# Performance work log

Measured on AMD Instinct MI355X. Metric: run time of the kernel, lower is better.

Reference implementation:

```python
import jax, jax.numpy as jnp
import numpy as np

N_NODES = 50000
N_EDGES = 600000
IN_F, HID, OUT_F = 602, 128, 41


def _gconv(x, W, b, src, dst, n):
    # DGL GraphConv, norm='both': D_dst^{-1/2} A (D_src^{-1/2} x W) + b
    ones = jnp.ones(src.shape, dtype=x.dtype)
    deg_out = jnp.clip(jax.ops.segment_sum(ones, src, num_segments=n), 1.0)
    deg_in = jnp.clip(jax.ops.segment_sum(ones, dst, num_segments=n), 1.0)
    h = x * jax.lax.rsqrt(deg_out)[:, None]
    h = h @ W  # dense transform first (in_feats > out_feats path)
    agg = jax.ops.segment_sum(h[src], dst, num_segments=n)  # [N, out]
    return agg * jax.lax.rsqrt(deg_in)[:, None] + b


def setup_inputs() -> dict:
    key = jax.random.key(0)
    ks = jax.random.split(key, 8)
    features = jax.random.normal(ks[0], (N_NODES, IN_F), dtype=jnp.float32)
    src = jax.random.randint(ks[1], (N_EDGES,), 0, N_NODES, dtype=jnp.int32)
    dst = jax.random.randint(ks[2], (N_EDGES,), 0, N_NODES, dtype=jnp.int32)
    def glorot(k, fan_in, fan_out):
        s = jnp.sqrt(6.0 / (fan_in + fan_out)).astype(jnp.float32)
        return jax.random.uniform(k, (fan_in, fan_out), jnp.float32, -s, s)
    return {
        'features': features, 'src': src, 'dst': dst,
        'W1': glorot(ks[3], IN_F, HID), 'b1': jnp.zeros((HID,), jnp.float32),
        'W2': glorot(ks[4], HID, HID), 'b2': jnp.zeros((HID,), jnp.float32),
        'W3': glorot(ks[5], HID, HID), 'b3': jnp.zeros((HID,), jnp.float32),
        'Wfc': glorot(ks[6], HID, OUT_F), 'bfc': jnp.zeros((OUT_F,), jnp.float32),
    }


def reference(features, src, dst, W1, b1, W2, b2, W3, b3, Wfc, bfc):
    n = features.shape[0]
    relu = jax.nn.relu
    x = relu(_gconv(features, W1, b1, src, dst, n))  # x = _x
    _x = relu(_gconv(x, W2, b2, src, dst, n))        # branch (layer2)
    x = relu(_gconv(x, W2, b2, src, dst, n))         # main (same layer2)
    x = relu(_gconv(x, W3, b3, src, dst, n))         # layer3
    x = relu(x + _x)                                  # residual + relu
    return x @ Wfc + bfc
```

## Files before the change

### kernel.cpp

```cpp
#include <hip/hip_runtime.h>
#include <hip/hip_bf16.h>

#define NN   50000
#define NE   600000
#define INF  602
#define HID  128
#define OUTF 41
#define NBLK 196

typedef __attribute__((ext_vector_type(8))) short bf16x8;
typedef __attribute__((ext_vector_type(4))) float f32x4;

__device__ inline unsigned short f2bf(float x) {
    unsigned u = __float_as_uint(x);
    unsigned r = u + 0x7FFF + ((u >> 16) & 1);
    return (unsigned short)(r >> 16);
}

#define GLL16(gp, lp) \
    __builtin_amdgcn_global_load_lds((const __attribute__((address_space(1))) unsigned int*)(gp), \
                                     (__attribute__((address_space(3))) unsigned int*)(lp), 16, 0, 0)

__global__ __launch_bounds__(256) void deg_hist_k(const int* __restrict__ src,
                                                  const int* __restrict__ dst,
                                                  int* __restrict__ cnt_out,
                                                  int* __restrict__ cnt_in, int E) {
    int e = blockIdx.x * 256 + threadIdx.x;
    if (e < E) {
        atomicAdd(&cnt_out[src[e]], 1);
        atomicAdd(&cnt_in[dst[e]], 1);
    }
}

__global__ __launch_bounds__(256) void scan1_k(const int* __restrict__ cnt,
                                               int* __restrict__ rowptr,
                                               int* __restrict__ blockSum) {
    __shared__ int tmp[256];
    int tid = threadIdx.x;
    int i = blockIdx.x * 256 + tid;
    int v = (i < NN) ? cnt[i] : 0;
    tmp[tid] = v;
    __syncthreads();
#pragma unroll
    for (int off = 1; off < 256; off <<= 1) {
        int t = (tid >= off) ? tmp[tid - off] : 0;
        __syncthreads();
        tmp[tid] += t;
        __syncthreads();
    }
    if (i < NN) rowptr[i] = tmp[tid] - v;
    if (tid == 255) blockSum[blockIdx.x] = tmp[255];
}

__global__ __launch_bounds__(256) void scan2_k(const int* __restrict__ blockSum,
                                               int* __restrict__ blockOff,
                                               int* __restrict__ rowptr) {
    __shared__ int tmp[256];
    int tid = threadIdx.x;
    int v = (tid < NBLK) ? blockSum[tid] : 0;
    tmp[tid] = v;
    __syncthreads();
#pragma unroll
    for (int off = 1; off < 256; off <<= 1) {
        int t = (tid >= off) ? tmp[tid - off] : 0;
        __syncthreads();
        tmp[tid] += t;
        __syncthreads();
    }
    if (tid < NBLK) blockOff[tid] = tmp[tid] - v;
    if (tid == 255) rowptr[NN] = tmp[255];
}

__global__ __launch_bounds__(256) void scan3_k(int* __restrict__ rowptr,
                                               const int* __restrict__ blockOff,
                                               int* __restrict__ wcur,
                                               const int* __restrict__ cnt_out,
                                               const int* __restrict__ cnt_in,
                                               float* __restrict__ rs_out,
                                               float* __restrict__ rs_in) {
    int i = blockIdx.x * 256 + threadIdx.x;
    if (i < NN) {
        int r = rowptr[i] + blockOff[blockIdx.x];
        rowptr[i] = r;
        wcur[i] = r;
        int co = cnt_out[i]; if (co < 1) co = 1;
        int ci = cnt_in[i];  if (ci < 1) ci = 1;
        rs_out[i] = rsqrtf((float)co);
        rs_in[i]  = rsqrtf((float)ci);
    }
}

__global__ __launch_bounds__(256) void fill_csr_k(const int* __restrict__ src,
                                                  const int* __restrict__ dst,
                                                  int* __restrict__ wcur,
                                                  int* __restrict__ csrsrc, int E) {
    int e = blockIdx.x * 256 + threadIdx.x;
    if (e < E) {
        int p = atomicAdd(&wcur[dst[e]], 1);
        csrsrc[p] = src[e];
    }
}

__device__ inline void prep_w_body(const float* __restrict__ W, int K,
                                   unsigned short* __restrict__ out, int total4, int i) {
    if (i >= total4) return;
    int col = i & 127;
    int k4 = (i >> 7) << 2;
    short4 h;
    h.x = (short)f2bf((k4 + 0 < K) ? W[(size_t)(k4 + 0) * HID + col] : 0.f);
    h.y = (short)f2bf((k4 + 1 < K) ? W[(size_t)(k4 + 1) * HID + col] : 0.f);
    h.z = (short)f2bf((k4 + 2 < K) ? W[(size_t)(k4 + 2) * HID + col] : 0.f);
    h.w = (short)f2bf((k4 + 3 < K) ? W[(size_t)(k4 + 3) * HID + col] : 0.f);
    *(short4*)&out[(size_t)(k4 >> 3) * 1024 + col * 8 + (k4 & 7)] = h;
}

__global__ __launch_bounds__(256) void prep_w_k(const float* __restrict__ W, int K,
                                                unsigned short* __restrict__ out, int total4) {
    prep_w_body(W, K, out, total4, blockIdx.x * 256 + threadIdx.x);
}

__global__ __launch_bounds__(256) void prep_w2_k(const float* __restrict__ Wa,
                                                 unsigned short* __restrict__ outa,
                                                 const float* __restrict__ Wb,
                                                 unsigned short* __restrict__ outb) {
    if (blockIdx.x < 16)
        prep_w_body(Wa, HID, outa, 4096, blockIdx.x * 256 + threadIdx.x);
    else
        prep_w_body(Wb, HID, outb, 4096, (blockIdx.x - 16) * 256 + threadIdx.x);
}

__global__ __launch_bounds__(256) void gemm1_k(const float* __restrict__ A,
                                               const unsigned short* __restrict__ Wt,
                                               const float* __restrict__ rs_out,
                                               unsigned short* __restrict__ H, int n) {
    __shared__ __attribute__((aligned(16))) short As[64 * 136];
    __shared__ __attribute__((aligned(16))) short Bs[16 * 1024];

    const int tid = threadIdx.x;
    const int wave = tid >> 6;
    const int lane = tid & 63;
    const int quad = lane >> 4;
    const int l16 = lane & 15;
    const int rowBase = blockIdx.x * 64;
    const int tileBase = rowBase + wave * 16;

    float4 apf[8];
    auto loadA = [&](int ch) {
        int kb = ch * 128;
#pragma unroll
        for (int c = 0; c < 8; ++c) {
            int f = c * 256 + tid;
            int row = f >> 5;
            int kc = (f & 31) << 2;
            int grow = rowBase + row;
            int gk = kb + kc;
            float4 v = {0.f, 0.f, 0.f, 0.f};
            if (grow < n) {
                if (gk + 3 < INF) {
                    v = *(const float4*)(A + (size_t)grow * INF + gk);
                } else {
                    if (gk + 0 < INF) v.x = A[(size_t)grow * INF + gk + 0];
                    if (gk + 1 < INF) v.y = A[(size_t)grow * INF + gk + 1];
                    if (gk + 2 < INF) v.z = A[(size_t)grow * INF + gk + 2];
                }
            }
            apf[c] = v;
        }
    };
    auto storeA = [&]() {
#pragma unroll
        for (int c = 0; c < 8; ++c) {
            int f = c * 256 + tid;
            int row = f >> 5;
            int kc = (f & 31) << 2;
            short4 h;
            h.x = (short)f2bf(apf[c].x); h.y = (short)f2bf(apf[c].y);
            h.z = (short)f2bf(apf[c].z); h.w = (short)f2bf(apf[c].w);
            *(short4*)&As[row * 136 + kc] = h;
        }
    };
    auto issueB = [&](int ch) {
#pragma unroll
        for (int c = 0; c < 8; ++c)
            GLL16(Wt + (size_t)ch * 16384 + c * 2048 + tid * 8, &Bs[c * 2048 + tid * 8]);
    };

    f32x4 acc[8];
#pragma unroll
    for (int j = 0; j < 8; ++j) acc[j] = (f32x4){0.f, 0.f, 0.f, 0.f};

    loadA(0);
    for (int ch = 0; ch < 5; ++ch) {
        __syncthreads();
        issueB(ch);
        storeA();
        __syncthreads();
        if (ch + 1 < 5) loadA(ch + 1);
#pragma unroll
        for (int s = 0; s < 4; ++s) {
            bf16x8 af = *(const bf16x8*)&As[(wave * 16 + l16) * 136 + s * 32 + quad * 8];
            const short* bg = &Bs[(s * 4 + quad) * 1024 + l16 * 8];
#pragma unroll
            for (int nt = 0; nt < 8; ++nt) {
                bf16x8 bf = *(const bf16x8*)(bg + nt * 128);
                acc[nt] = __builtin_amdgcn_mfma_f32_16x16x32_bf16(af, bf, acc[nt], 0, 0, 0);
            }
        }
    }

#pragma unroll
    for (int r = 0; r < 4; ++r) {
        int row = tileBase + quad * 4 + r;
        if (row < n) {
            float ro = rs_out[row];
#pragma unroll
            for (int nt = 0; nt < 8; ++nt)
                H[(size_t)row * HID + nt * 16 + l16] = f2bf(acc[nt][r] * ro);
        }
    }
}

__global__ __launch_bounds__(256) void gemm_hid_k(const unsigned short* __restrict__ A,
                                                  const unsigned short* __restrict__ Wt,
                                                  unsigned short* __restrict__ H, int n) {
    __shared__ __attribute__((aligned(16))) short As[64 * 136];
    __shared__ __attribute__((aligned(16))) short Bs[16384];

    const int tid = threadIdx.x;
    const int wave = tid >> 6;
    const int lane = tid & 63;
    const int quad = lane >> 4;
    const int l16 = lane & 15;
    const int wm = wave >> 1;
    const int wn = wave & 1;
    const int rowBase = blockIdx.x * 64;

#pragma unroll
    for (int c = 0; c < 8; ++c)
        GLL16(Wt + c * 2048 + tid * 8, &Bs[c * 2048 + tid * 8]);

#pragma unroll
    for (int c = 0; c < 4; ++c) {
        int f = c * 256 + tid;
        int row = f >> 4;
        int k16 = (f & 15) << 3;
        int grow = rowBase + row;
        int4 v = {0, 0, 0, 0};
        if (grow < n) v = *(const int4*)(A + (size_t)grow * HID + k16);
        *(int4*)&As[row * 136 + k16] = v;
    }
    __syncthreads();

    f32x4 acc[2][4];
#pragma unroll
    for (int i = 0; i < 2; ++i)
#pragma unroll
        for (int j = 0; j < 4; ++j) acc[i][j] = (f32x4){0.f, 0.f, 0.f, 0.f};

#pragma unroll
    for (int kq = 0; kq < 4; ++kq) {
        bf16x8 af[2], bfr[4];
#pragma unroll
        for (int mt = 0; mt < 2; ++mt)
            af[mt] = *(const bf16x8*)&As[(wm * 32 + mt * 16 + l16) * 136 + kq * 32 + quad * 8];
#pragma unroll
        for (int nt = 0; nt < 4; ++nt)
            bfr[nt] = *(const bf16x8*)&Bs[(kq * 4 + quad) * 1024 + (wn * 64 + nt * 16 + l16) * 8];
#pragma unroll
        for (int mt = 0; mt < 2; ++mt)
#pragma unroll
            for (int nt = 0; nt < 4; ++nt)
                acc[mt][nt] = __builtin_amdgcn_mfma_f32_16x16x32_bf16(af[mt], bfr[nt], acc[mt][nt], 0, 0, 0);
    }

#pragma unroll
    for (int mt = 0; mt < 2; ++mt)
#pragma unroll
        for (int r = 0; r < 4; ++r) {
            int row = rowBase + wm * 32 + mt * 16 + quad * 4 + r;
            if (row < n) {
#pragma unroll
                for (int nt = 0; nt < 4; ++nt) {
                    int col = wn * 64 + nt * 16 + l16;
                    H[(size_t)row * HID + col] = f2bf(acc[mt][nt][r]);
                }
            }
        }
}

__global__ __launch_bounds__(256) void gather_k(const unsigned short* __restrict__ H,
                                                const int* __restrict__ rowptr,
                                                const int* __restrict__ csrsrc,
                                                const float* __restrict__ rs_in,
                                                const float* __restrict__ rs_out,
                                                const float* __restrict__ bias,
                                                const float* __restrict__ resid,
                                                float* __restrict__ outX,
                                                unsigned short* __restrict__ outXs,
                                                int n) {
    const int lane = threadIdx.x & 63;
    const int g = lane >> 4;
    const int l = lane & 15;
    const int gbase = g << 4;
    const int wid = blockIdx.x * 4 + (threadIdx.x >> 6);
    const int node = wid * 4 + g;
    const bool alive = node < n;

    int beg = 0, end = 0;
    if (alive) { beg = rowptr[node]; end = rowptr[node + 1]; }

    float acc[8];
#pragma unroll
    for (int k = 0; k < 8; ++k) acc[k] = 0.f;

    auto accum = [&](int s) {
        int4 u = *(const int4*)(H + (size_t)s * HID + l * 8);
        unsigned x = (unsigned)u.x, y = (unsigned)u.y, z = (unsigned)u.z, w = (unsigned)u.w;
        acc[0] += __uint_as_float(x << 16); acc[1] += __uint_as_float(x & 0xFFFF0000u);
        acc[2] += __uint_as_float(y << 16); acc[3] += __uint_as_float(y & 0xFFFF0000u);
        acc[4] += __uint_as_float(z << 16); acc[5] += __uint_as_float(z & 0xFFFF0000u);
        acc[6] += __uint_as_float(w << 16); acc[7] += __uint_as_float(w & 0xFFFF0000u);
    };

    for (int base = beg; base < end; base += 16) {
        int m = end - base; if (m > 16) m = 16;
        int idx = (l < m) ? csrsrc[base + l] : 0;
        int j = 0;
        for (; j + 3 < m; j += 4) {
            int s0 = __shfl(idx, gbase | j);
            int s1 = __shfl(idx, gbase | (j + 1));
            int s2 = __shfl(idx, gbase | (j + 2));
            int s3 = __shfl(idx, gbase | (j + 3));
            int4 u0 = *(const int4*)(H + (size_t)s0 * HID + l * 8);
            int4 u1 = *(const int4*)(H + (size_t)s1 * HID + l * 8);
            int4 u2 = *(const int4*)(H + (size_t)s2 * HID + l * 8);
            int4 u3 = *(const int4*)(H + (size_t)s3 * HID + l * 8);
#pragma unroll
            for (int q = 0; q < 4; ++q) {
                int4 u = (q == 0) ? u0 : (q == 1) ? u1 : (q == 2) ? u2 : u3;
                unsigned x = (unsigned)u.x, y = (unsigned)u.y, z = (unsigned)u.z, w = (unsigned)u.w;
                acc[0] += __uint_as_float(x << 16); acc[1] += __uint_as_float(x & 0xFFFF0000u);
                acc[2] += __uint_as_float(y << 16); acc[3] += __uint_as_float(y & 0xFFFF0000u);
                acc[4] += __uint_as_float(z << 16); acc[5] += __uint_as_float(z & 0xFFFF0000u);
                acc[6] += __uint_as_float(w << 16); acc[7] += __uint_as_float(w & 0xFFFF0000u);
            }
        }
        for (; j < m; ++j) accum(__shfl(idx, gbase | j));
    }

    if (!alive) return;

    float ri = rs_in[node];
    float4 b0 = *(const float4*)(bias + l * 8);
    float4 b1 = *(const float4*)(bias + l * 8 + 4);
    float v[8];
    v[0] = fmaxf(acc[0] * ri + b0.x, 0.f); v[1] = fmaxf(acc[1] * ri + b0.y, 0.f);
    v[2] = fmaxf(acc[2] * ri + b0.z, 0.f); v[3] = fmaxf(acc[3] * ri + b0.w, 0.f);
    v[4] = fmaxf(acc[4] * ri + b1.x, 0.f); v[5] = fmaxf(acc[5] * ri + b1.y, 0.f);
    v[6] = fmaxf(acc[6] * ri + b1.z, 0.f); v[7] = fmaxf(acc[7] * ri + b1.w, 0.f);

    size_t o = (size_t)node * HID + l * 8;
    if (resid) {
        float4 r0 = *(const float4*)(resid + o);
        float4 r1 = *(const float4*)(resid + o + 4);
        v[0] = fmaxf(v[0] + r0.x, 0.f); v[1] = fmaxf(v[1] + r0.y, 0.f);
        v[2] = fmaxf(v[2] + r0.z, 0.f); v[3] = fmaxf(v[3] + r0.w, 0.f);
        v[4] = fmaxf(v[4] + r1.x, 0.f); v[5] = fmaxf(v[5] + r1.y, 0.f);
        v[6] = fmaxf(v[6] + r1.z, 0.f); v[7] = fmaxf(v[7] + r1.w, 0.f);
    }
    if (outX) {
        *(float4*)(outX + o) = make_float4(v[0], v[1], v[2], v[3]);
        *(float4*)(outX + o + 4) = make_float4(v[4], v[5], v[6], v[7]);
    }
    if (outXs) {
        float ro = rs_out[node];
        int4 h;
        h.x = (int)(((unsigned)f2bf(v[1] * ro) << 16) | f2bf(v[0] * ro));
        h.y = (int)(((unsigned)f2bf(v[3] * ro) << 16) | f2bf(v[2] * ro));
        h.z = (int)(((unsigned)f2bf(v[5] * ro) << 16) | f2bf(v[4] * ro));
        h.w = (int)(((unsigned)f2bf(v[7] * ro) << 16) | f2bf(v[6] * ro));
        *(int4*)(outXs + o) = h;
    }
}

__global__ __launch_bounds__(256) void fc_k(const float* __restrict__ X,
                                            const float* __restrict__ Wfc,
                                            const float* __restrict__ bfc,
                                            float* __restrict__ out, int n) {
    __shared__ float Ws[HID * OUTF];
    __shared__ float Xs[4][HID];
    int tid = threadIdx.x;
    for (int i = tid; i < HID * OUTF; i += 256) Ws[i] = Wfc[i];
    int rowBase = blockIdx.x * 4;
    for (int i = tid; i < 4 * HID; i += 256) {
        int r = i >> 7, c = i & 127;
        int gr = rowBase + r;
        Xs[r][c] = (gr < n) ? X[(size_t)gr * HID + c] : 0.f;
    }
    __syncthreads();
    int wv = tid >> 6, lane = tid & 63;
    int row = rowBase + wv;
    if (row < n && lane < OUTF) {
        float acc = bfc[lane];
#pragma unroll 8
        for (int k = 0; k < HID; ++k) acc += Xs[wv][k] * Ws[k * OUTF + lane];
        out[(size_t)row * OUTF + lane] = acc;
    }
}

extern "C" void kernel_launch(void* const* d_in, const int* in_sizes, int n_in,
                              void* d_out, int out_size, void* d_ws, size_t ws_size,
                              hipStream_t stream) {
    const float* feat = (const float*)d_in[0];
    const int* src = (const int*)d_in[1];
    const int* dst = (const int*)d_in[2];
    const float* W1 = (const float*)d_in[3];
    const float* b1 = (const float*)d_in[4];
    const float* W2 = (const float*)d_in[5];
    const float* b2 = (const float*)d_in[6];
    const float* W3 = (const float*)d_in[7];
    const float* b3 = (const float*)d_in[8];
    const float* Wfc = (const float*)d_in[9];
    const float* bfc = (const float*)d_in[10];
    float* out = (float*)d_out;

    char* w = (char*)d_ws;
    auto alloc = [&](size_t b) -> void* {
        void* p = (void*)w;
        w += (b + 255) & ~(size_t)255;
        return p;
    };
    int* cnt = (int*)alloc(2 * NN * sizeof(int));
    int* cnt_out = cnt;
    int* cnt_in  = cnt + NN;
    int* rowptr  = (int*)alloc((NN + 1) * sizeof(int));
    int* wcur    = (int*)alloc(NN * sizeof(int));
    int* csrsrc  = (int*)alloc(NE * sizeof(int));
    int* blockSum = (int*)alloc(NBLK * sizeof(int));
    int* blockOff = (int*)alloc(NBLK * sizeof(int));
    float* rs_out = (float*)alloc(NN * sizeof(float));
    float* rs_in  = (float*)alloc(NN * sizeof(float));
    unsigned short* W1t = (unsigned short*)alloc(10 * 8192 * sizeof(unsigned short));
    unsigned short* W2t = (unsigned short*)alloc(16384 * sizeof(unsigned short));
    unsigned short* W3t = (unsigned short*)alloc(16384 * sizeof(unsigned short));
    unsigned short* Hb = (unsigned short*)alloc((size_t)NN * HID * sizeof(unsigned short));
    unsigned short* Xb = (unsigned short*)alloc((size_t)NN * HID * sizeof(unsigned short));
    float* resid = (float*)alloc((size_t)NN * HID * sizeof(float));
    float* Xfc   = (float*)alloc((size_t)NN * HID * sizeof(float));

    hipMemsetAsync(cnt, 0, 2 * NN * sizeof(int), stream);

    prep_w_k<<<80, 256, 0, stream>>>(W1, INF, W1t, 20480);
    prep_w2_k<<<32, 256, 0, stream>>>(W2, W2t, W3, W3t);

    deg_hist_k<<<(NE + 255) / 256, 256, 0, stream>>>(src, dst, cnt_out, cnt_in, NE);
    scan1_k<<<NBLK, 256, 0, stream>>>(cnt_in, rowptr, blockSum);
    scan2_k<<<1, 256, 0, stream>>>(blockSum, blockOff, rowptr);
    scan3_k<<<NBLK, 256, 0, stream>>>(rowptr, blockOff, wcur, cnt_out, cnt_in, rs_out, rs_in);
    fill_csr_k<<<(NE + 255) / 256, 256, 0, stream>>>(src, dst, wcur, csrsrc, NE);

    const int gblk = (NN + 63) / 64;
    const int ablk = (NN + 15) / 16;
    gemm1_k<<<gblk, 256, 0, stream>>>(feat, W1t, rs_out, Hb, NN);
    gather_k<<<ablk, 256, 0, stream>>>(Hb, rowptr, csrsrc, rs_in, rs_out, b1,
                                       nullptr, nullptr, Xb, NN);
    gemm_hid_k<<<gblk, 256, 0, stream>>>(Xb, W2t, Hb, NN);
    gather_k<<<ablk, 256, 0, stream>>>(Hb, rowptr, csrsrc, rs_in, rs_out, b2,
                                       nullptr, resid, Xb, NN);
    gemm_hid_k<<<gblk, 256, 0, stream>>>(Xb, W3t, Hb, NN);
    gather_k<<<ablk, 256, 0, stream>>>(Hb, rowptr, csrsrc, rs_in, rs_out, b3,
                                       resid, Xfc, nullptr, NN);
    fc_k<<<(NN + 3) / 4, 256, 0, stream>>>(Xfc, Wfc, bfc, out, NN);
}
```

Measured before the change: 455.7 us.

## Fuse neighbor gather into following GEMM and final FC; merge scan and prep kernels

Each gather/aggregation stage is fused with the next dense transform. The aggregated, normalized bf16 rows are written straight into the GEMM's LDS tile instead of round-tripping through global memory. The last gather is fused with the residual add and the 41-wide FC layer, which drops the fp32 Xfc buffer. The two-level scan's second and third kernels are merged, with each block reducing blockSum itself, and the weight prep and memset are merged into one kernel, cutting launches. The costs are lower parallelism in the gather phase (64 rows per block, 4 passes per wave) and more LDS per block, which may lower occupancy.

```diff
diff --git a/kernel.cpp b/kernel.cpp
--- a/kernel.cpp
+++ b/kernel.cpp
@@ -52,35 +52,30 @@
     if (tid == 255) blockSum[blockIdx.x] = tmp[255];
 }
 
-__global__ __launch_bounds__(256) void scan2_k(const int* __restrict__ blockSum,
-                                               int* __restrict__ blockOff,
-                                               int* __restrict__ rowptr) {
-    __shared__ int tmp[256];
-    int tid = threadIdx.x;
-    int v = (tid < NBLK) ? blockSum[tid] : 0;
-    tmp[tid] = v;
+__global__ __launch_bounds__(256) void scan23_k(int* __restrict__ rowptr,
+                                                const int* __restrict__ blockSum,
+                                                int* __restrict__ wcur,
+                                                const int* __restrict__ cnt_out,
+                                                const int* __restrict__ cnt_in,
+                                                float* __restrict__ rs_out,
+                                                float* __restrict__ rs_in) {
+    const int tid = threadIdx.x;
+    const int bid = blockIdx.x;
+    int vAll = (tid < NBLK) ? blockSum[tid] : 0;
+    int vPre = (tid < bid) ? vAll : 0;
+#pragma unroll
+    for (int o = 32; o; o >>= 1) {
+        vAll += __shfl_down(vAll, o);
+        vPre += __shfl_down(vPre, o);
+    }
+    __shared__ int sA[4], sP[4];
+    if ((tid & 63) == 0) { sA[tid >> 6] = vAll; sP[tid >> 6] = vPre; }
     __syncthreads();
-#pragma unroll
-    for (int off = 1; off < 256; off <<= 1) {
-        int t = (tid >= off) ? tmp[tid - off] : 0;
-        __syncthreads();
-        tmp[tid] += t;
-        __syncthreads();
-    }
-    if (tid < NBLK) blockOff[tid] = tmp[tid] - v;
-    if (tid == 255) rowptr[NN] = tmp[255];
-}
-
-__global__ __launch_bounds__(256) void scan3_k(int* __restrict__ rowptr,
-                                               const int* __restrict__ blockOff,
-                                               int* __restrict__ wcur,
-                                               const int* __restrict__ cnt_out,
-                                               const int* __restrict__ cnt_in,
-                                               float* __restrict__ rs_out,
-                                               float* __restrict__ rs_in) {
-    int i = blockIdx.x * 256 + threadIdx.x;
+    int offAll = sA[0] + sA[1] + sA[2] + sA[3];
+    int offPre = sP[0] + sP[1] + sP[2] + sP[3];
+    int i = bid * 256 + tid;
     if (i < NN) {
-        int r = rowptr[i] + blockOff[blockIdx.x];
+        int r = rowptr[i] + offPre;
         rowptr[i] = r;
         wcur[i] = r;
         int co = cnt_out[i]; if (co < 1) co = 1;
@@ -88,6 +83,7 @@
         rs_out[i] = rsqrtf((float)co);
         rs_in[i]  = rsqrtf((float)ci);
     }
+    if (bid == NBLK - 1 && tid == 0) rowptr[NN] = offAll;
 }
 
 __global__ __launch_bounds__(256) void fill_csr_k(const int* __restrict__ src,
@@ -114,19 +110,23 @@
     *(short4*)&out[(size_t)(k4 >> 3) * 1024 + col * 8 + (k4 & 7)] = h;
 }
 
-__global__ __launch_bounds__(256) void prep_w_k(const float* __restrict__ W, int K,
-                                                unsigned short* __restrict__ out, int total4) {
-    prep_w_body(W, K, out, total4, blockIdx.x * 256 + threadIdx.x);
-}
-
-__global__ __launch_bounds__(256) void prep_w2_k(const float* __restrict__ Wa,
-                                                 unsigned short* __restrict__ outa,
-                                                 const float* __restrict__ Wb,
-                                                 unsigned short* __restrict__ outb) {
-    if (blockIdx.x < 16)
-        prep_w_body(Wa, HID, outa, 4096, blockIdx.x * 256 + threadIdx.x);
-    else
-        prep_w_body(Wb, HID, outb, 4096, (blockIdx.x - 16) * 256 + threadIdx.x);
+__global__ __launch_bounds__(256) void prep_all_k(const float* __restrict__ W1,
+                                                  const float* __restrict__ W2,
+                                                  const float* __restrict__ W3,
+                                                  unsigned short* __restrict__ W1t,
+                                                  unsigned short* __restrict__ W2t,
+                                                  unsigned short* __restrict__ W3t,
+                                                  int* __restrict__ cnt) {
+    int b = blockIdx.x;
+    if (b < 80) {
+        int t = b * 256 + threadIdx.x;
+        prep_w_body(W1, INF, W1t, 20480, t);
+        for (int i = t; i < 2 * NN; i += 20480) cnt[i] = 0;
+    } else if (b < 96) {
+        prep_w_body(W2, HID, W2t, 4096, (b - 80) * 256 + threadIdx.x);
+    } else {
+        prep_w_body(W3, HID, W3t, 4096, (b - 96) * 256 + threadIdx.x);
+    }
 }
 
 __global__ __launch_bounds__(256) void gemm1_k(const float* __restrict__ A,
@@ -220,124 +220,68 @@
     }
 }
 
-__global__ __launch_bounds__(256) void gemm_hid_k(const unsigned short* __restrict__ A,
-                                                  const unsigned short* __restrict__ Wt,
-                                                  unsigned short* __restrict__ H, int n) {
+__global__ __launch_bounds__(256) void fgath_gemm_k(const unsigned short* __restrict__ Hin,
+                                                    const unsigned short* __restrict__ Wt,
+                                                    const int* __restrict__ rowptr,
+                                                    const int* __restrict__ csrsrc,
+                                                    const float* __restrict__ rs_in,
+                                                    const float* __restrict__ rs_out,
+                                                    const float* __restrict__ bias,
+                                                    float* __restrict__ resid,
+                                                    unsigned short* __restrict__ Hout,
+                                                    int n) {
     __shared__ __attribute__((aligned(16))) short As[64 * 136];
     __shared__ __attribute__((aligned(16))) short Bs[16384];
 
     const int tid = threadIdx.x;
     const int wave = tid >> 6;
     const int lane = tid & 63;
-    const int quad = lane >> 4;
-    const int l16 = lane & 15;
-    const int wm = wave >> 1;
-    const int wn = wave & 1;
-    const int rowBase = blockIdx.x * 64;
-
-#pragma unroll
-    for (int c = 0; c < 8; ++c)
-        GLL16(Wt + c * 2048 + tid * 8, &Bs[c * 2048 + tid * 8]);
-
-#pragma unroll
-    for (int c = 0; c < 4; ++c) {
-        int f = c * 256 + tid;
-        int row = f >> 4;
-        int k16 = (f & 15) << 3;
-        int grow = rowBase + row;
-        int4 v = {0, 0, 0, 0};
-        if (grow < n) v = *(const int4*)(A + (size_t)grow * HID + k16);
-        *(int4*)&As[row * 136 + k16] = v;
-    }
-    __syncthreads();
-
-    f32x4 acc[2][4];
-#pragma unroll
-    for (int i = 0; i < 2; ++i)
-#pragma unroll
-        for (int j = 0; j < 4; ++j) acc[i][j] = (f32x4){0.f, 0.f, 0.f, 0.f};
-
-#pragma unroll
-    for (int kq = 0; kq < 4; ++kq) {
-        bf16x8 af[2], bfr[4];
-#pragma unroll
-        for (int mt = 0; mt < 2; ++mt)
-            af[mt] = *(const bf16x8*)&As[(wm * 32 + mt * 16 + l16) * 136 + kq * 32 + quad * 8];
-#pragma unroll
-        for (int nt = 0; nt < 4; ++nt)
-            bfr[nt] = *(const bf16x8*)&Bs[(kq * 4 + quad) * 1024 + (wn * 64 + nt * 16 + l16) * 8];
-#pragma unroll
-        for (int mt = 0; mt < 2; ++mt)
-#pragma unroll
-            for (int nt = 0; nt < 4; ++nt)
-                acc[mt][nt] = __builtin_amdgcn_mfma_f32_16x16x32_bf16(af[mt], bfr[nt], acc[mt][nt], 0, 0, 0);
-    }
-
-#pragma unroll
-    for (int mt = 0; mt < 2; ++mt)
-#pragma unroll
-        for (int r = 0; r < 4; ++r) {
-            int row = rowBase + wm * 32 + mt * 16 + quad * 4 + r;
-            if (row < n) {
-#pragma unroll
-                for (int nt = 0; nt < 4; ++nt) {
-                    int col = wn * 64 + nt * 16 + l16;
-                    H[(size_t)row * HID + col] = f2bf(acc[mt][nt][r]);
-                }
-            }
-        }
-}
-
-__global__ __launch_bounds__(256) void gather_k(const unsigned short* __restrict__ H,
-                                                const int* __restrict__ rowptr,
-                                                const int* __restrict__ csrsrc,
-                                                const float* __restrict__ rs_in,
-                                                const float* __restrict__ rs_out,
-                                                const float* __restrict__ bias,
-                                                const float* __restrict__ resid,
-                                                float* __restrict__ outX,
-                                                unsigned short* __restrict__ outXs,
-                                                int n) {
-    const int lane = threadIdx.x & 63;
     const int g = lane >> 4;
     const int l = lane & 15;
     const int gbase = g << 4;
-    const int wid = blockIdx.x * 4 + (threadIdx.x >> 6);
-    const int node = wid * 4 + g;
-    const bool alive = node < n;
-
-    int beg = 0, end = 0;
-    if (alive) { beg = rowptr[node]; end = rowptr[node + 1]; }
-
-    float acc[8];
-#pragma unroll
-    for (int k = 0; k < 8; ++k) acc[k] = 0.f;
-
-    auto accum = [&](int s) {
-        int4 u = *(const int4*)(H + (size_t)s * HID + l * 8);
-        unsigned x = (unsigned)u.x, y = (unsigned)u.y, z = (unsigned)u.z, w = (unsigned)u.w;
-        acc[0] += __uint_as_float(x << 16); acc[1] += __uint_as_float(x & 0xFFFF0000u);
-        acc[2] += __uint_as_float(y << 16); acc[3] += __uint_as_float(y & 0xFFFF0000u);
-        acc[4] += __uint_as_float(z << 16); acc[5] += __uint_as_float(z & 0xFFFF0000u);
-        acc[6] += __uint_as_float(w << 16); acc[7] += __uint_as_float(w & 0xFFFF0000u);
-    };
-
-    for (int base = beg; base < end; base += 16) {
-        int m = end - base; if (m > 16) m = 16;
-        int idx = (l < m) ? csrsrc[base + l] : 0;
-        int j = 0;
-        for (; j + 3 < m; j += 4) {
-            int s0 = __shfl(idx, gbase | j);
-            int s1 = __shfl(idx, gbase | (j + 1));
-            int s2 = __shfl(idx, gbase | (j + 2));
-            int s3 = __shfl(idx, gbase | (j + 3));
-            int4 u0 = *(const int4*)(H + (size_t)s0 * HID + l * 8);
-            int4 u1 = *(const int4*)(H + (size_t)s1 * HID + l * 8);
-            int4 u2 = *(const int4*)(H + (size_t)s2 * HID + l * 8);
-            int4 u3 = *(const int4*)(H + (size_t)s3 * HID + l * 8);
-#pragma unroll
-            for (int q = 0; q < 4; ++q) {
-                int4 u = (q == 0) ? u0 : (q == 1) ? u1 : (q == 2) ? u2 : u3;
+    const int rowBase = blockIdx.x * 64;
+
+#pragma unroll
+    for (int c = 0; c < 8; ++c)
+        GLL16(Wt + c * 2048 + tid * 8, &Bs[c * 2048 + tid * 8]);
+
+    for (int p = 0; p < 4; ++p) {
+        int lrow = wave * 16 + p * 4 + g;
+        int node = rowBase + lrow;
+        bool alive = node < n;
+        int beg = 0, end = 0;
+        if (alive) { beg = rowptr[node]; end = rowptr[node + 1]; }
+
+        float acc[8];
+#pragma unroll
+        for (int k = 0; k < 8; ++k) acc[k] = 0.f;
+
+        for (int base = beg; base < end; base += 16) {
+            int m = end - base; if (m > 16) m = 16;
+            int idx = (l < m) ? csrsrc[base + l] : 0;
+            int j = 0;
+            for (; j + 3 < m; j += 4) {
+                int s0 = __shfl(idx, gbase | j);
+                int s1 = __shfl(idx, gbase | (j + 1));
+                int s2 = __shfl(idx, gbase | (j + 2));
+                int s3 = __shfl(idx, gbase | (j + 3));
+                int4 u0 = *(const int4*)(Hin + (size_t)s0 * HID + l * 8);
+                int4 u1 = *(const int4*)(Hin + (size_t)s1 * HID + l * 8);
+                int4 u2 = *(const int4*)(Hin + (size_t)s2 * HID + l * 8);
+                int4 u3 = *(const int4*)(Hin + (size_t)s3 * HID + l * 8);
+#pragma unroll
+                for (int q = 0; q < 4; ++q) {
+                    int4 u = (q == 0) ? u0 : (q == 1) ? u1 : (q == 2) ? u2 : u3;
+                    unsigned x = (unsigned)u.x, y = (unsigned)u.y, z = (unsigned)u.z, w = (unsigned)u.w;
+                    acc[0] += __uint_as_float(x << 16); acc[1] += __uint_as_float(x & 0xFFFF0000u);
+                    acc[2] += __uint_as_float(y << 16); acc[3] += __uint_as_float(y & 0xFFFF0000u);
+                    acc[4] += __uint_as_float(z << 16); acc[5] += __uint_as_float(z & 0xFFFF0000u);
+                    acc[6] += __uint_as_float(w << 16); acc[7] += __uint_as_float(w & 0xFFFF0000u);
+                }
+            }
+            for (; j < m; ++j) {
+                int s = __shfl(idx, gbase | j);
+                int4 u = *(const int4*)(Hin + (size_t)s * HID + l * 8);
                 unsigned x = (unsigned)u.x, y = (unsigned)u.y, z = (unsigned)u.z, w = (unsigned)u.w;
                 acc[0] += __uint_as_float(x << 16); acc[1] += __uint_as_float(x & 0xFFFF0000u);
                 acc[2] += __uint_as_float(y << 16); acc[3] += __uint_as_float(y & 0xFFFF0000u);
@@ -345,66 +289,184 @@
                 acc[6] += __uint_as_float(w << 16); acc[7] += __uint_as_float(w & 0xFFFF0000u);
             }
         }
-        for (; j < m; ++j) accum(__shfl(idx, gbase | j));
-    }
-
-    if (!alive) return;
-
-    float ri = rs_in[node];
-    float4 b0 = *(const float4*)(bias + l * 8);
-    float4 b1 = *(const float4*)(bias + l * 8 + 4);
-    float v[8];
-    v[0] = fmaxf(acc[0] * ri + b0.x, 0.f); v[1] = fmaxf(acc[1] * ri + b0.y, 0.f);
-    v[2] = fmaxf(acc[2] * ri + b0.z, 0.f); v[3] = fmaxf(acc[3] * ri + b0.w, 0.f);
-    v[4] = fmaxf(acc[4] * ri + b1.x, 0.f); v[5] = fmaxf(acc[5] * ri + b1.y, 0.f);
-    v[6] = fmaxf(acc[6] * ri + b1.z, 0.f); v[7] = fmaxf(acc[7] * ri + b1.w, 0.f);
-
-    size_t o = (size_t)node * HID + l * 8;
-    if (resid) {
-        float4 r0 = *(const float4*)(resid + o);
-        float4 r1 = *(const float4*)(resid + o + 4);
-        v[0] = fmaxf(v[0] + r0.x, 0.f); v[1] = fmaxf(v[1] + r0.y, 0.f);
-        v[2] = fmaxf(v[2] + r0.z, 0.f); v[3] = fmaxf(v[3] + r0.w, 0.f);
-        v[4] = fmaxf(v[4] + r1.x, 0.f); v[5] = fmaxf(v[5] + r1.y, 0.f);
-        v[6] = fmaxf(v[6] + r1.z, 0.f); v[7] = fmaxf(v[7] + r1.w, 0.f);
-    }
-    if (outX) {
-        *(float4*)(outX + o) = make_float4(v[0], v[1], v[2], v[3]);
-        *(float4*)(outX + o + 4) = make_float4(v[4], v[5], v[6], v[7]);
-    }
-    if (outXs) {
-        float ro = rs_out[node];
-        int4 h;
-        h.x = (int)(((unsigned)f2bf(v[1] * ro) << 16) | f2bf(v[0] * ro));
-        h.y = (int)(((unsigned)f2bf(v[3] * ro) << 16) | f2bf(v[2] * ro));
-        h.z = (int)(((unsigned)f2bf(v[5] * ro) << 16) | f2bf(v[4] * ro));
-        h.w = (int)(((unsigned)f2bf(v[7] * ro) << 16) | f2bf(v[6] * ro));
-        *(int4*)(outXs + o) = h;
-    }
-}
-
-__global__ __launch_bounds__(256) void fc_k(const float* __restrict__ X,
-                                            const float* __restrict__ Wfc,
-                                            const float* __restrict__ bfc,
-                                            float* __restrict__ out, int n) {
+
+        if (alive) {
+            float ri = rs_in[node];
+            float4 b0 = *(const float4*)(bias + l * 8);
+            float4 b1 = *(const float4*)(bias + l * 8 + 4);
+            float v[8];
+            v[0] = fmaxf(acc[0] * ri + b0.x, 0.f); v[1] = fmaxf(acc[1] * ri + b0.y, 0.f);
+            v[2] = fmaxf(acc[2] * ri + b0.z, 0.f); v[3] = fmaxf(acc[3] * ri + b0.w, 0.f);
+            v[4] = fmaxf(acc[4] * ri + b1.x, 0.f); v[5] = fmaxf(acc[5] * ri + b1.y, 0.f);
+            v[6] = fmaxf(acc[6] * ri + b1.z, 0.f); v[7] = fmaxf(acc[7] * ri + b1.w, 0.f);
+            if (resid) {
+                size_t o = (size_t)node * HID + l * 8;
+                *(float4*)(resid + o) = make_float4(v[0], v[1], v[2], v[3]);
+                *(float4*)(resid + o + 4) = make_float4(v[4], v[5], v[6], v[7]);
+            }
+            float ro = rs_out[node];
+            int4 h;
+            h.x = (int)(((unsigned)f2bf(v[1] * ro) << 16) | f2bf(v[0] * ro));
+            h.y = (int)(((unsigned)f2bf(v[3] * ro) << 16) | f2bf(v[2] * ro));
+            h.z = (int)(((unsigned)f2bf(v[5] * ro) << 16) | f2bf(v[4] * ro));
+            h.w = (int)(((unsigned)f2bf(v[7] * ro) << 16) | f2bf(v[6] * ro));
+            *(int4*)&As[lrow * 136 + l * 8] = h;
+        } else {
+            *(int4*)&As[lrow * 136 + l * 8] = make_int4(0, 0, 0, 0);
+        }
+    }
+    __syncthreads();
+
+    const int quad = lane >> 4;
+    const int l16 = lane & 15;
+    const int wm = wave >> 1;
+    const int wn = wave & 1;
+
+    f32x4 acc2[2][4];
+#pragma unroll
+    for (int i = 0; i < 2; ++i)
+#pragma unroll
+        for (int j = 0; j < 4; ++j) acc2[i][j] = (f32x4){0.f, 0.f, 0.f, 0.f};
+
+#pragma unroll
+    for (int kq = 0; kq < 4; ++kq) {
+        bf16x8 af[2], bfr[4];
+#pragma unroll
+        for (int mt = 0; mt < 2; ++mt)
+            af[mt] = *(const bf16x8*)&As[(wm * 32 + mt * 16 + l16) * 136 + kq * 32 + quad * 8];
+#pragma unroll
+        for (int nt = 0; nt < 4; ++nt)
+            bfr[nt] = *(const bf16x8*)&Bs[(kq * 4 + quad) * 1024 + (wn * 64 + nt * 16 + l16) * 8];
+#pragma unroll
+        for (int mt = 0; mt < 2; ++mt)
+#pragma unroll
+            for (int nt = 0; nt < 4; ++nt)
+                acc2[mt][nt] = __builtin_amdgcn_mfma_f32_16x16x32_bf16(af[mt], bfr[nt], acc2[mt][nt], 0, 0, 0);
+    }
+
+#pragma unroll
+    for (int mt = 0; mt < 2; ++mt)
+#pragma unroll
+        for (int r = 0; r < 4; ++r) {
+            int row = rowBase + wm * 32 + mt * 16 + quad * 4 + r;
+            if (row < n) {
+#pragma unroll
+                for (int nt = 0; nt < 4; ++nt) {
+                    int col = wn * 64 + nt * 16 + l16;
+                    Hout[(size_t)row * HID + col] = f2bf(acc2[mt][nt][r]);
+                }
+            }
+        }
+}
+
+__global__ __launch_bounds__(256) void ffc_k(const unsigned short* __restrict__ Hin,
+                                             const int* __restrict__ rowptr,
+                                             const int* __restrict__ csrsrc,
+                                             const float* __restrict__ rs_in,
+                                             const float* __restrict__ bias,
+                                             const float* __restrict__ resid,
+                                             const float* __restrict__ Wfc,
+                                             const float* __restrict__ bfc,
+                                             float* __restrict__ out, int n) {
+    __shared__ float Xs[64][HID];
     __shared__ float Ws[HID * OUTF];
-    __shared__ float Xs[4][HID];
-    int tid = threadIdx.x;
+
+    const int tid = threadIdx.x;
+    const int wave = tid >> 6;
+    const int lane = tid & 63;
+    const int g = lane >> 4;
+    const int l = lane & 15;
+    const int gbase = g << 4;
+    const int rowBase = blockIdx.x * 64;
+
     for (int i = tid; i < HID * OUTF; i += 256) Ws[i] = Wfc[i];
-    int rowBase = blockIdx.x * 4;
-    for (int i = tid; i < 4 * HID; i += 256) {
-        int r = i >> 7, c = i & 127;
-        int gr = rowBase + r;
-        Xs[r][c] = (gr < n) ? X[(size_t)gr * HID + c] : 0.f;
+
+    for (int p = 0; p < 4; ++p) {
+        int lrow = wave * 16 + p * 4 + g;
+        int node = rowBase + lrow;
+        bool alive = node < n;
+        int beg = 0, end = 0;
+        if (alive) { beg = rowptr[node]; end = rowptr[node + 1]; }
+
+        float acc[8];
+#pragma unroll
+        for (int k = 0; k < 8; ++k) acc[k] = 0.f;
+
+        for (int base = beg; base < end; base += 16) {
+            int m = end - base; if (m > 16) m = 16;
+            int idx = (l < m) ? csrsrc[base + l] : 0;
+            int j = 0;
+            for (; j + 3 < m; j += 4) {
+                int s0 = __shfl(idx, gbase | j);
+                int s1 = __shfl(idx, gbase | (j + 1));
+                int s2 = __shfl(idx, gbase | (j + 2));
+                int s3 = __shfl(idx, gbase | (j + 3));
+                int4 u0 = *(const int4*)(Hin + (size_t)s0 * HID + l * 8);
+                int4 u1 = *(const int4*)(Hin + (size_t)s1 * HID + l * 8);
+                int4 u2 = *(const int4*)(Hin + (size_t)s2 * HID + l * 8);
+                int4 u3 = *(const int4*)(Hin + (size_t)s3 * HID + l * 8);
+#pragma unroll
+                for (int q = 0; q < 4; ++q) {
+                    int4 u = (q == 0) ? u0 : (q == 1) ? u1 : (q == 2) ? u2 : u3;
+                    unsigned x = (unsigned)u.x, y = (unsigned)u.y, z = (unsigned)u.z, w = (unsigned)u.w;
+                    acc[0] += __uint_as_float(x << 16); acc[1] += __uint_as_float(x & 0xFFFF0000u);
+                    acc[2] += __uint_as_float(y << 16); acc[3] += __uint_as_float(y & 0xFFFF0000u);
+                    acc[4] += __uint_as_float(z << 16); acc[5] += __uint_as_float(z & 0xFFFF0000u);
+                    acc[6] += __uint_as_float(w << 16); acc[7] += __uint_as_float(w & 0xFFFF0000u);
+                }
+            }
+            for (; j < m; ++j) {
+                int s = __shfl(idx, gbase | j);
+                int4 u = *(const int4*)(Hin + (size_t)s * HID + l * 8);
+                unsigned x = (unsigned)u.x, y = (unsigned)u.y, z = (unsigned)u.z, w = (unsigned)u.w;
+                acc[0] += __uint_as_float(x << 16); acc[1] += __uint_as_float(x & 0xFFFF0000u);
+                acc[2] += __uint_as_float(y << 16); acc[3] += __uint_as_float(y & 0xFFFF0000u);
+                acc[4] += __uint_as_float(z << 16); acc[5] += __uint_as_float(z & 0xFFFF0000u);
+                acc[6] += __uint_as_float(w << 16); acc[7] += __uint_as_float(w & 0xFFFF0000u);
+            }
+        }
+
+        if (alive) {
+            float ri = rs_in[node];
+            float4 b0 = *(const float4*)(bias + l * 8);
+            float4 b1 = *(const float4*)(bias + l * 8 + 4);
+            size_t o = (size_t)node * HID + l * 8;
+            float4 r0 = *(const float4*)(resid + o);
+            float4 r1 = *(const float4*)(resid + o + 4);
+            float v[8];
+            v[0] = fmaxf(fmaxf(acc[0] * ri + b0.x, 0.f) + r0.x, 0.f);
+            v[1] = fmaxf(fmaxf(acc[1] * ri + b0.y, 0.f) + r0.y, 0.f);
+            v[2] = fmaxf(fmaxf(acc[2] * ri + b0.z, 0.f) + r0.z, 0.f);
+            v[3] = fmaxf(fmaxf(acc[3] * ri + b0.w, 0.f) + r0.w, 0.f);
+            v[4] = fmaxf(fmaxf(acc[4] * ri + b1.x, 0.f) + r1.x, 0.f);
+            v[5] = fmaxf(fmaxf(acc[5] * ri + b1.y, 0.f) + r1.y, 0.f);
+            v[6] = fmaxf(fmaxf(acc[6] * ri + b1.z, 0.f) + r1.z, 0.f);
+            v[7] = fmaxf(fmaxf(acc[7] * ri + b1.w, 0.f) + r1.w, 0.f);
+            *(float4*)&Xs[lrow][l * 8]     = make_float4(v[0], v[1], v[2], v[3]);
+            *(float4*)&Xs[lrow][l * 8 + 4] = make_float4(v[4], v[5], v[6], v[7]);
+        } else {
+            *(float4*)&Xs[lrow][l * 8]     = make_float4(0.f, 0.f, 0.f, 0.f);
+            *(float4*)&Xs[lrow][l * 8 + 4] = make_float4(0.f, 0.f, 0.f, 0.f);
+        }
     }
     __syncthreads();
-    int wv = tid >> 6, lane = tid & 63;
-    int row = rowBase + wv;
-    if (row < n && lane < OUTF) {
-        float acc = bfc[lane];
-#pragma unroll 8
-        for (int k = 0; k < HID; ++k) acc += Xs[wv][k] * Ws[k * OUTF + lane];
-        out[(size_t)row * OUTF + lane] = acc;
+
+    float bb = (lane < OUTF) ? bfc[lane] : 0.f;
+    for (int r = 0; r < 16; ++r) {
+        int lrow = wave * 16 + r;
+        int row = rowBase + lrow;
+        if (row < n && lane < OUTF) {
+            float a = bb;
+#pragma unroll 4
+            for (int k = 0; k < HID; k += 4) {
+                float4 xv = *(const float4*)&Xs[lrow][k];
+                a += xv.x * Ws[(k + 0) * OUTF + lane];
+                a += xv.y * Ws[(k + 1) * OUTF + lane];
+                a += xv.z * Ws[(k + 2) * OUTF + lane];
+                a += xv.w * Ws[(k + 3) * OUTF + lane];
+            }
+            out[(size_t)row * OUTF + lane] = a;
+        }
     }
 }
 
@@ -437,38 +499,26 @@
     int* wcur    = (int*)alloc(NN * sizeof(int));
     int* csrsrc  = (int*)alloc(NE * sizeof(int));
     int* blockSum = (int*)alloc(NBLK * sizeof(int));
-    int* blockOff = (int*)alloc(NBLK * sizeof(int));
     float* rs_out = (float*)alloc(NN * sizeof(float));
     float* rs_in  = (float*)alloc(NN * sizeof(float));
     unsigned short* W1t = (unsigned short*)alloc(10 * 8192 * sizeof(unsigned short));
     unsigned short* W2t = (unsigned short*)alloc(16384 * sizeof(unsigned short));
     unsigned short* W3t = (unsigned short*)alloc(16384 * sizeof(unsigned short));
-    unsigned short* Hb = (unsigned short*)alloc((size_t)NN * HID * sizeof(unsigned short));
-    unsigned short* Xb = (unsigned short*)alloc((size_t)NN * HID * sizeof(unsigned short));
+    unsigned short* Ha = (unsigned short*)alloc((size_t)NN * HID * sizeof(unsigned short));
+    unsigned short* Hc = (unsigned short*)alloc((size_t)NN * HID * sizeof(unsigned short));
     float* resid = (float*)alloc((size_t)NN * HID * sizeof(float));
-    float* Xfc   = (float*)alloc((size_t)NN * HID * sizeof(float));
-
-    hipMemsetAsync(cnt, 0, 2 * NN * sizeof(int), stream);
-
-    prep_w_k<<<80, 256, 0, stream>>>(W1, INF, W1t, 20480);
-    prep_w2_k<<<32, 256, 0, stream>>>(W2, W2t, W3, W3t);
-
+
+    prep_all_k<<<112, 256, 0, stream>>>(W1, W2, W3, W1t, W2t, W3t, cnt);
     deg_hist_k<<<(NE + 255) / 256, 256, 0, stream>>>(src, dst, cnt_out, cnt_in, NE);
     scan1_k<<<NBLK, 256, 0, stream>>>(cnt_in, rowptr, blockSum);
-    scan2_k<<<1, 256, 0, stream>>>(blockSum, blockOff, rowptr);
-    scan3_k<<<NBLK, 256, 0, stream>>>(rowptr, blockOff, wcur, cnt_out, cnt_in, rs_out, rs_in);
+    scan23_k<<<NBLK, 256, 0, stream>>>(rowptr, blockSum, wcur, cnt_out, cnt_in, rs_out, rs_in);
     fill_csr_k<<<(NE + 255) / 256, 256, 0, stream>>>(src, dst, wcur, csrsrc, NE);
 
     const int gblk = (NN + 63) / 64;
-    const int ablk = (NN + 15) / 16;
-    gemm1_k<<<gblk, 256, 0, stream>>>(feat, W1t, rs_out, Hb, NN);
-    gather_k<<<ablk, 256, 0, stream>>>(Hb, rowptr, csrsrc, rs_in, rs_out, b1,
-                                       nullptr, nullptr, Xb, NN);
-    gemm_hid_k<<<gblk, 256, 0, stream>>>(Xb, W2t, Hb, NN);
-    gather_k<<<ablk, 256, 0, stream>>>(Hb, rowptr, csrsrc, rs_in, rs_out, b2,
-                                       nullptr, resid, Xb, NN);
-    gemm_hid_k<<<gblk, 256, 0, stream>>>(Xb, W3t, Hb, NN);
-    gather_k<<<ablk, 256, 0, stream>>>(Hb, rowptr, csrsrc, rs_in, rs_out, b3,
-                                       resid, Xfc, nullptr, NN);
-    fc_k<<<(NN + 3) / 4, 256, 0, stream>>>(Xfc, Wfc, bfc, out, NN);
-}
+    gemm1_k<<<gblk, 256, 0, stream>>>(feat, W1t, rs_out, Ha, NN);
+    fgath_gemm_k<<<gblk, 256, 0, stream>>>(Ha, W2t, rowptr, csrsrc, rs_in, rs_out, b1,
+                                           nullptr, Hc, NN);
+    fgath_gemm_k<<<gblk, 256, 0, stream>>>(Hc, W3t, rowptr, csrsrc, rs_in, rs_out, b2,
+                                           resid, Ha, NN);
+    ffc_k<<<gblk, 256, 0, stream>>>(Ha, rowptr, csrsrc, rs_in, b3, resid, Wfc, bfc, out, NN);
+}
```

Measured after the change: 481.3 us. +5.6%, slower.
